# Performance work log

Measured on AMD Instinct MI355X. Metric: run time of the kernel, lower is better.

The kernel has to match this reference:

```python
import jax, jax.numpy as jnp
import numpy as np

B, CQ, CVK, L, H = 4, 256, 256, 2048, 8
D = CVK // H  # depth per head = 32
EPS = 1e-5    # BatchNorm eps


def setup_inputs() -> dict:
    key = jax.random.key(0)
    ks = jax.random.split(key, 32)
    n = lambda i, s, sc=1.0: jax.random.normal(ks[i], s, dtype=jnp.float32) * sc
    u = lambda i, s: jax.random.uniform(ks[i], s, dtype=jnp.float32, minval=0.5, maxval=1.5)
    inp = {
        'v': n(0, (B, CVK, L)), 'k': n(1, (B, CVK, L)), 'q': n(2, (B, CQ, L)),
        # trainable positional encodings (pe_q: image_shape_q, pe_vk: image_shape_vk)
        'pe_q': n(3, (CQ, L)), 'pe_vk': n(4, (CVK, L)),
        # W_query / W_key / W_value: Conv1d(kernel=1) weight [out,in] + bias, then BatchNorm1d (eval mode)
        'wq': n(5, (CVK, CQ), 0.05), 'bq': n(6, (CVK,), 0.05),
        'gq': 1.0 + n(7, (CVK,), 0.1), 'betaq': n(8, (CVK,), 0.1), 'mq': n(9, (CVK,), 0.1), 'varq': u(10, (CVK,)),
        'wk': n(11, (CVK, CVK), 0.05), 'bk': n(12, (CVK,), 0.05),
        'gk': 1.0 + n(13, (CVK,), 0.1), 'betak': n(14, (CVK,), 0.1), 'mk': n(15, (CVK,), 0.1), 'vark': u(16, (CVK,)),
        'wv': n(17, (CVK, CVK), 0.05), 'bv': n(18, (CVK,), 0.05),
        'gv': 1.0 + n(19, (CVK,), 0.1), 'betav': n(20, (CVK,), 0.1), 'mv': n(21, (CVK,), 0.1), 'varv': u(22, (CVK,)),
        # out_proj (zero-init in original; randomized here so gradients are non-trivial)
        'wo': n(23, (CQ, CVK), 0.05), 'bo': n(24, (CQ,), 0.05),
    }
    return inp


def _conv1(x, w, b):  # 1x1 conv == channel matmul: [b,c,l] -> [b,o,l]
    return jnp.einsum('oc,bcl->bol', w, x) + b[None, :, None]


def _bn(x, g, beta, mean, var):  # eval-mode BatchNorm1d over channel dim
    scale = g / jnp.sqrt(var + EPS)
    return (x - mean[:, None]) * scale[:, None] + beta[:, None]


def _mha(v, k, q, pe_q, pe_vk, wq, bq, gq, betaq, mq, varq,
         wk, bk, gk, betak, mk, vark, wv, bv, gv, betav, mv, varv, wo, bo):
    q_orig = q
    b = q.shape[0]
    vv = v + pe_vk[None]
    kk = k + pe_vk[None]
    qq = q + pe_q[None]
    qp = _bn(_conv1(qq, wq, bq), gq, betaq, mq, varq)   # [b, CVK, L]
    kp = _bn(_conv1(kk, wk, bk), gk, betak, mk, vark)
    vp = _bn(_conv1(vv, wv, bv), gv, betav, mv, varv)
    # split heads: [b, H, D, L]
    qh = qp.reshape(b, H, D, -1)
    kh = kp.reshape(b, H, D, -1)
    vh = vp.reshape(b, H, D, -1)
    # scaled dot-product attention over sequence dim (l: query pos, m: key pos)
    scores = jnp.einsum('bhdl,bhdm->bhlm', qh, kh) / jnp.sqrt(jnp.float32(D))
    p = jax.nn.softmax(scores, axis=-1)
    a = jnp.einsum('bhlm,bhdm->bhdl', p, vh)            # [b, H, D, L]
    a = a.reshape(b, H * D, -1)                          # [b, CVK, L]
    out = _conv1(a, wo, bo)                              # [b, CQ, L]
    return q_orig + out


def reference(v, k, q, pe_q, pe_vk, wq, bq, gq, betaq, mq, varq,
              wk, bk, gk, betak, mk, vark, wv, bv, gv, betav, mv, varv, wo, bo):
    return _mha(v, k, q, pe_q, pe_vk, wq, bq, gq, betaq, mq, varq,
                wk, bk, gk, betak, mk, vark, wv, bv, gv, betav, mv, varv, wo, bo)
```

## Files before the change

### kernel.cpp

```cpp
#include <hip/hip_runtime.h>
#include <hip/hip_bf16.h>

#define BB 4
#define CC 256
#define LL 2048
#define HH 8
#define DD 32
#define EPSV 1e-5f

typedef __bf16 bf16x8 __attribute__((ext_vector_type(8)));
typedef __bf16 bf16x4 __attribute__((ext_vector_type(4)));
typedef __bf16 bf16x2 __attribute__((ext_vector_type(2)));
typedef float  f32x4  __attribute__((ext_vector_type(4)));
typedef float  f32x16 __attribute__((ext_vector_type(16)));
typedef unsigned int u32x4 __attribute__((ext_vector_type(4)));

static __device__ __forceinline__ unsigned pkbf(float lo, float hi) {
    bf16x2 p; p[0] = (__bf16)lo; p[1] = (__bf16)hi;
    return __builtin_bit_cast(unsigned, p);
}

__global__ __launch_bounds__(256) void prep_kernel(
    const float* __restrict__ qin, const float* __restrict__ kin,
    const float* __restrict__ vin, const float* __restrict__ peq,
    const float* __restrict__ pevk,
    __bf16* __restrict__ xq, __bf16* __restrict__ xk, __bf16* __restrict__ xv,
    const float* __restrict__ wq, const float* __restrict__ bq,
    const float* __restrict__ gq, const float* __restrict__ betaq,
    const float* __restrict__ mq, const float* __restrict__ varq,
    const float* __restrict__ wk, const float* __restrict__ bk,
    const float* __restrict__ gk, const float* __restrict__ betak,
    const float* __restrict__ mk, const float* __restrict__ vark,
    const float* __restrict__ wv, const float* __restrict__ bv,
    const float* __restrict__ gv, const float* __restrict__ betav,
    const float* __restrict__ mv, const float* __restrict__ varv,
    const float* __restrict__ wo,
    __bf16* __restrict__ wqb, __bf16* __restrict__ wkb,
    __bf16* __restrict__ wvb, __bf16* __restrict__ wob,
    float* __restrict__ bqf, float* __restrict__ bkf, float* __restrict__ bvf,
    float qscale)
{
    __shared__ __align__(16) float xs[64][66];
    const int t = threadIdx.x;

    if (blockIdx.z == 12) {
        const int which = blockIdx.y;
        const float* w    = which==0?wq:(which==1?wk:(which==2?wv:wo));
        const float* bias = which==0?bq:(which==1?bk:bv);
        const float* g    = which==0?gq:(which==1?gk:gv);
        const float* beta = which==0?betaq:(which==1?betak:betav);
        const float* mean = which==0?mq:(which==1?mk:mv);
        const float* var  = which==0?varq:(which==1?vark:varv);
        __bf16* wout = which==0?wqb:(which==1?wkb:(which==2?wvb:wob));
        float*  bout = which==0?bqf:(which==1?bkf:bvf);
        const float extra = (which==0) ? qscale : 1.0f;

        const int base = blockIdx.x * 2048;
        for (int i = 0; i < 8; ++i) {
            const int idx = base + i * 256 + t;
            const int o = idx >> 8;
            const float sc = (which < 3) ? (g[o] * rsqrtf(var[o] + EPSV) * extra) : 1.0f;
            wout[idx] = (__bf16)(w[idx] * sc);
        }
        if (blockIdx.x == 0 && which < 3) {
            const int o = t;
            const float sc = g[o] * rsqrtf(var[o] + EPSV);
            bout[o] = ((bias[o] - mean[o]) * sc + beta[o]) * extra;
        }
        return;
    }

    const int lt = blockIdx.x * 64;
    const int ct = blockIdx.y * 64;
    const int z  = blockIdx.z;
    const int b  = z & 3;
    const int which = z >> 2;

    const float* xin = which == 0 ? qin : (which == 1 ? kin : vin);
    const float* pe  = which == 0 ? peq : pevk;
    __bf16* xout     = which == 0 ? xq  : (which == 1 ? xk : xv);

    for (int i = 0; i < 8; ++i) {
        const int idx = i * 256 + t;
        const int row = idx >> 5;
        const int lch = idx & 31;
        const float2 xv2 = *(const float2*)&xin[(size_t)(b * CC + ct + row) * LL + lt + lch * 2];
        const float2 pv2 = *(const float2*)&pe[(size_t)(ct + row) * LL + lt + lch * 2];
        float2 s; s.x = xv2.x + pv2.x; s.y = xv2.y + pv2.y;
        *(float2*)&xs[row][lch * 2] = s;
    }
    __syncthreads();

    for (int i = 0; i < 2; ++i) {
        const int idx = i * 256 + t;
        const int lrow = idx >> 3;
        const int ch   = idx & 7;
        bf16x8 v;
        #pragma unroll
        for (int j = 0; j < 8; ++j) v[j] = (__bf16)xs[ch * 8 + j][lrow];
        *(bf16x8*)&xout[(size_t)(b * LL + lt + lrow) * CC + ct + ch * 8] = v;
    }
}

__global__ __launch_bounds__(512) void qkv_gemm_kernel(
    const __bf16* __restrict__ wqb, const __bf16* __restrict__ wkb,
    const __bf16* __restrict__ wvb,
    const __bf16* __restrict__ xq, const __bf16* __restrict__ xk,
    const __bf16* __restrict__ xv,
    const float* __restrict__ bqf, const float* __restrict__ bkf,
    const float* __restrict__ bvf,
    __bf16* __restrict__ qTo, __bf16* __restrict__ kTo, __bf16* __restrict__ vNo)
{
    __shared__ __align__(16) __bf16 Wl[64][136];
    __shared__ __align__(16) __bf16 Xl[128][136];
    __bf16 (*Tl)[72] = (__bf16(*)[72])Xl;

    const int z = blockIdx.z;
    const int which = z >> 2;
    const int b = z & 3;
    const __bf16* W    = which==0 ? wqb : (which==1 ? wkb : wvb);
    const __bf16* X    = which==0 ? xq  : (which==1 ? xk  : xv);
    const float*  bias = which==0 ? bqf : (which==1 ? bkf : bvf);

    const int lt = blockIdx.x * 128;
    const int ot = blockIdx.y * 64;
    const int t  = threadIdx.x;
    const int wv = t >> 6;
    const int wm = wv >> 2;
    const int wn = wv & 3;
    const int l  = t & 63;
    const int lq = l & 15;
    const int g  = l >> 4;

    f32x4 acc[2][2];
    #pragma unroll
    for (int mi = 0; mi < 2; ++mi)
        #pragma unroll
        for (int ni = 0; ni < 2; ++ni) acc[mi][ni] = (f32x4){0.f,0.f,0.f,0.f};

    for (int ks = 0; ks < 2; ++ks) {
        __syncthreads();
        #pragma unroll
        for (int i = 0; i < 2; ++i) {
            const int idx = i * 512 + t;
            const int row = idx >> 4, ch = idx & 15;
            *(bf16x8*)&Wl[row][ch * 8] =
                *(const bf16x8*)&W[(size_t)(ot + row) * CC + ks * 128 + ch * 8];
        }
        #pragma unroll
        for (int i = 0; i < 4; ++i) {
            const int idx = i * 512 + t;
            const int row = idx >> 4, ch = idx & 15;
            *(bf16x8*)&Xl[row][ch * 8] =
                *(const bf16x8*)&X[(size_t)(b * LL + lt + row) * CC + ks * 128 + ch * 8];
        }
        __syncthreads();

        #pragma unroll
        for (int kk = 0; kk < 4; ++kk) {
            bf16x8 af[2], bfr[2];
            #pragma unroll
            for (int mi = 0; mi < 2; ++mi)
                af[mi] = *(const bf16x8*)&Wl[wm * 32 + mi * 16 + lq][kk * 32 + g * 8];
            #pragma unroll
            for (int ni = 0; ni < 2; ++ni)
                bfr[ni] = *(const bf16x8*)&Xl[wn * 32 + ni * 16 + lq][kk * 32 + g * 8];
            #pragma unroll
            for (int mi = 0; mi < 2; ++mi)
                #pragma unroll
                for (int ni = 0; ni < 2; ++ni)
                    acc[mi][ni] = __builtin_amdgcn_mfma_f32_16x16x32_bf16(
                        af[mi], bfr[ni], acc[mi][ni], 0, 0, 0);
        }
    }

    if (which < 2) {
        __bf16* outT = which==0 ? qTo : kTo;
        __syncthreads();
        #pragma unroll
        for (int mi = 0; mi < 2; ++mi) {
            const float4 b4 = *(const float4*)&bias[ot + wm * 32 + mi * 16 + g * 4];
            #pragma unroll
            for (int ni = 0; ni < 2; ++ni) {
                bf16x4 pv;
                pv[0] = (__bf16)(acc[mi][ni][0] + b4.x);
                pv[1] = (__bf16)(acc[mi][ni][1] + b4.y);
                pv[2] = (__bf16)(acc[mi][ni][2] + b4.z);
                pv[3] = (__bf16)(acc[mi][ni][3] + b4.w);
                *(bf16x4*)&Tl[wn * 32 + ni * 16 + lq][wm * 32 + mi * 16 + g * 4] = pv;
            }
        }
        __syncthreads();
        #pragma unroll
        for (int i = 0; i < 2; ++i) {
            const int idx = i * 512 + t;
            const int lrow = idx >> 3, ch = idx & 7;
            *(bf16x8*)&outT[(size_t)(b * LL + lt + lrow) * CC + ot + ch * 8] =
                *(const bf16x8*)&Tl[lrow][ch * 8];
        }
    } else {
        #pragma unroll
        for (int mi = 0; mi < 2; ++mi) {
            const float4 b4 = *(const float4*)&bias[ot + wm * 32 + mi * 16 + g * 4];
            const float bb[4] = {b4.x, b4.y, b4.z, b4.w};
            #pragma unroll
            for (int ni = 0; ni < 2; ++ni) {
                const int col = lt + wn * 32 + ni * 16 + lq;
                #pragma unroll
                for (int r = 0; r < 4; ++r) {
                    const int o = ot + wm * 32 + mi * 16 + g * 4 + r;
                    vNo[(size_t)(b * CC + o) * LL + col] = (__bf16)(acc[mi][ni][r] + bb[r]);
                }
            }
        }
    }
}

__global__ __launch_bounds__(256) void attn_mfma_kernel(
    const __bf16* __restrict__ qT, const __bf16* __restrict__ kT,
    const __bf16* __restrict__ vN, __bf16* __restrict__ aT)
{
    __shared__ __align__(16) __bf16 KB[2][128 * 32];
    __shared__ __align__(16) __bf16 VB[2][32 * 128];

    const int qb = blockIdx.x;
    const int h  = blockIdx.y;
    const int b  = blockIdx.z;
    const int t  = threadIdx.x;
    const int w  = t >> 6;
    const int l  = t & 63;
    const int lq = l & 31;
    const int hi = l >> 5;

    const int q0 = qb * 128 + w * 32;

    const __bf16* qrow = qT + ((size_t)(b * LL) + q0 + lq) * CC + h * DD;
    const bf16x8 qf0 = *(const bf16x8*)&qrow[hi * 8];
    const bf16x8 qf1 = *(const bf16x8*)&qrow[16 + hi * 8];

    const __bf16* kTb = kT + (size_t)(b * LL) * CC + h * DD;
    const __bf16* vNb = vN + ((size_t)(b * CC) + h * DD) * LL;

    const int s0 = t, s1 = 256 + t;
    const int sk0 = s0 >> 2, sp0 = s0 & 3;
    const int sk1 = s1 >> 2, sp1 = s1 & 3;
    const int sd0 = s0 >> 4, sv0 = s0 & 15;
    const int sd1 = s1 >> 4, sv1 = s1 & 15;
    const int kw0 = sk0 * 32 + (sp0 ^ ((sk0 >> 1) & 3)) * 8;
    const int kw1 = sk1 * 32 + (sp1 ^ ((sk1 >> 1) & 3)) * 8;
    const int vw0 = sd0 * 128 + (sv0 ^ (sd0 & 7)) * 8;
    const int vw1 = sd1 * 128 + (sv1 ^ (sd1 & 7)) * 8;

    bf16x8 kr0, kr1, vr0, vr1;
    #define LOADREGS(KT0) \
        kr0 = *(const bf16x8*)&kTb[(size_t)((KT0) + sk0) * CC + sp0 * 8]; \
        kr1 = *(const bf16x8*)&kTb[(size_t)((KT0) + sk1) * CC + sp1 * 8]; \
        vr0 = *(const bf16x8*)&vNb[(size_t)sd0 * LL + (KT0) + sv0 * 8];   \
        vr1 = *(const bf16x8*)&vNb[(size_t)sd1 * LL + (KT0) + sv1 * 8];
    #define WRITEBUF(BUF) \
        *(bf16x8*)&KB[BUF][kw0] = kr0; *(bf16x8*)&KB[BUF][kw1] = kr1; \
        *(bf16x8*)&VB[BUF][vw0] = vr0; *(bf16x8*)&VB[BUF][vw1] = vr1;

    LOADREGS(0)
    WRITEBUF(0)
    LOADREGS(128)

    f32x16 O;
    #pragma unroll
    for (int r = 0; r < 16; ++r) O[r] = 0.f;
    float ssum = 0.f;

    const int NT = LL / 128;
    for (int it = 0; it < NT; ++it) {
        const int buf = it & 1;
        __syncthreads();
        const __bf16* KBb = KB[buf];
        const __bf16* VBb = VB[buf];

        #pragma unroll
        for (int kb = 0; kb < 128; kb += 32) {
            const int key = kb + lq;
            const int ksw = (key >> 1) & 3;
            f32x16 S;
            #pragma unroll
            for (int r = 0; r < 16; ++r) S[r] = 0.f;
            {
                const bf16x8 kf0 = *(const bf16x8*)&KBb[key * 32 + ((hi    ) ^ ksw) * 8];
                const bf16x8 kf1 = *(const bf16x8*)&KBb[key * 32 + ((2 + hi) ^ ksw) * 8];
                __builtin_amdgcn_s_setprio(1);
                S = __builtin_amdgcn_mfma_f32_32x32x16_bf16(kf0, qf0, S, 0, 0, 0);
                S = __builtin_amdgcn_mfma_f32_32x32x16_bf16(kf1, qf1, S, 0, 0, 0);
                __builtin_amdgcn_s_setprio(0);
            }
            float e[16];
            #pragma unroll
            for (int r = 0; r < 16; ++r) e[r] = __builtin_amdgcn_exp2f(S[r]);
            float s = 0.f;
            #pragma unroll
            for (int r = 0; r < 16; r += 4) s += (e[r] + e[r+1]) + (e[r+2] + e[r+3]);
            ssum += s;
            unsigned a[8];
            #pragma unroll
            for (int i = 0; i < 8; ++i) a[i] = pkbf(e[2*i], e[2*i+1]);
            #pragma unroll
            for (int c = 0; c < 2; ++c) {
                unsigned w0 = a[4*c+0], w1 = a[4*c+1], w2 = a[4*c+2], w3 = a[4*c+3];
                asm volatile("v_permlane32_swap_b32 %0, %1" : "+v"(w0), "+v"(w2));
                asm volatile("v_permlane32_swap_b32 %0, %1" : "+v"(w1), "+v"(w3));
                u32x4 pv4 = {w0, w1, w2, w3};
                const bf16x8 pf = __builtin_bit_cast(bf16x8, pv4);
                const int slot = (kb >> 3) + 2 * c + hi;
                const bf16x8 vf = *(const bf16x8*)&VBb[lq * 128 + (slot ^ (lq & 7)) * 8];
                __builtin_amdgcn_s_setprio(1);
                O = __builtin_amdgcn_mfma_f32_32x32x16_bf16(vf, pf, O, 0, 0, 0);
                __builtin_amdgcn_s_setprio(0);
            }
        }

        if (it + 1 < NT) { WRITEBUF(buf ^ 1) }
        if (it + 2 < NT) { LOADREGS((it + 2) * 128) }
    }
    #undef LOADREGS
    #undef WRITEBUF

    ssum += __shfl_xor(ssum, 32);
    const float inv = 1.f / ssum;

    __bf16* arow = aT + ((size_t)(b * LL) + q0 + lq) * CC + h * DD;
    #pragma unroll
    for (int gi = 0; gi < 4; ++gi) {
        bf16x4 ov;
        #pragma unroll
        for (int r = 0; r < 4; ++r) ov[r] = (__bf16)(O[4*gi + r] * inv);
        *(bf16x4*)&arow[8 * gi + 4 * hi] = ov;
    }
}

__global__ __launch_bounds__(256) void outproj_kernel(
    const __bf16* __restrict__ W, const __bf16* __restrict__ X,
    const float* __restrict__ bias, const float* __restrict__ resid,
    float* __restrict__ outF)
{
    __shared__ __align__(16) __bf16 Wl[64][136];
    __shared__ __align__(16) __bf16 Xl[64][136];

    const int lt = blockIdx.x * 64;
    const int ot = blockIdx.y * 64;
    const int b  = blockIdx.z;
    const int t  = threadIdx.x;
    const int wv = t >> 6;
    const int wm = wv >> 1;
    const int wn = wv & 1;
    const int l  = t & 63;
    const int lq = l & 15;
    const int g  = l >> 4;

    f32x4 acc[2][2];
    #pragma unroll
    for (int mi = 0; mi < 2; ++mi)
        #pragma unroll
        for (int ni = 0; ni < 2; ++ni) acc[mi][ni] = (f32x4){0.f,0.f,0.f,0.f};

    for (int ks = 0; ks < 2; ++ks) {
        __syncthreads();
        #pragma unroll
        for (int i = 0; i < 4; ++i) {
            const int idx = i * 256 + t;
            const int row = idx >> 4, ch = idx & 15;
            *(bf16x8*)&Wl[row][ch * 8] =
                *(const bf16x8*)&W[(size_t)(ot + row) * CC + ks * 128 + ch * 8];
        }
        #pragma unroll
        for (int i = 0; i < 4; ++i) {
            const int idx = i * 256 + t;
            const int row = idx >> 4, ch = idx & 15;
            *(bf16x8*)&Xl[row][ch * 8] =
                *(const bf16x8*)&X[(size_t)(b * LL + lt + row) * CC + ks * 128 + ch * 8];
        }
        __syncthreads();

        #pragma unroll
        for (int kk = 0; kk < 4; ++kk) {
            bf16x8 af[2], bfr[2];
            #pragma unroll
            for (int mi = 0; mi < 2; ++mi)
                af[mi] = *(const bf16x8*)&Wl[wm * 32 + mi * 16 + lq][kk * 32 + g * 8];
            #pragma unroll
            for (int ni = 0; ni < 2; ++ni)
                bfr[ni] = *(const bf16x8*)&Xl[wn * 32 + ni * 16 + lq][kk * 32 + g * 8];
            #pragma unroll
            for (int mi = 0; mi < 2; ++mi)
                #pragma unroll
                for (int ni = 0; ni < 2; ++ni)
                    acc[mi][ni] = __builtin_amdgcn_mfma_f32_16x16x32_bf16(
                        af[mi], bfr[ni], acc[mi][ni], 0, 0, 0);
        }
    }

    #pragma unroll
    for (int mi = 0; mi < 2; ++mi) {
        const float4 b4 = *(const float4*)&bias[ot + wm * 32 + mi * 16 + g * 4];
        const float bb[4] = {b4.x, b4.y, b4.z, b4.w};
        #pragma unroll
        for (int ni = 0; ni < 2; ++ni) {
            const int col = lt + wn * 32 + ni * 16 + lq;
            #pragma unroll
            for (int r = 0; r < 4; ++r) {
                const int o = ot + wm * 32 + mi * 16 + g * 4 + r;
                const size_t a = (size_t)(b * CC + o) * LL + col;
                outF[a] = acc[mi][ni][r] + bb[r] + resid[a];
            }
        }
    }
}

extern "C" void kernel_launch(void* const* d_in, const int* in_sizes, int n_in,
                              void* d_out, int out_size, void* d_ws, size_t ws_size,
                              hipStream_t stream)
{
    const float* v     = (const float*)d_in[0];
    const float* k     = (const float*)d_in[1];
    const float* q     = (const float*)d_in[2];
    const float* pe_q  = (const float*)d_in[3];
    const float* pe_vk = (const float*)d_in[4];
    const float* wq    = (const float*)d_in[5];
    const float* bq    = (const float*)d_in[6];
    const float* gq    = (const float*)d_in[7];
    const float* betaq = (const float*)d_in[8];
    const float* mq    = (const float*)d_in[9];
    const float* varq  = (const float*)d_in[10];
    const float* wk    = (const float*)d_in[11];
    const float* bk    = (const float*)d_in[12];
    const float* gk    = (const float*)d_in[13];
    const float* betak = (const float*)d_in[14];
    const float* mk    = (const float*)d_in[15];
    const float* vark  = (const float*)d_in[16];
    const float* wv    = (const float*)d_in[17];
    const float* bv    = (const float*)d_in[18];
    const float* gv    = (const float*)d_in[19];
    const float* betav = (const float*)d_in[20];
    const float* mv    = (const float*)d_in[21];
    const float* varv  = (const float*)d_in[22];
    const float* wo    = (const float*)d_in[23];
    const float* bo    = (const float*)d_in[24];

    float* out = (float*)d_out;

    const size_t E = (size_t)BB * CC * LL;
    __bf16* xq  = (__bf16*)d_ws;
    __bf16* xk  = xq + E;
    __bf16* xv  = xk + E;
    __bf16* qT  = xv + E;
    __bf16* kT  = qT + E;
    __bf16* vN  = kT + E;
    __bf16* aT  = vN + E;
    __bf16* wqb = aT + E;
    __bf16* wkb = wqb + 65536;
    __bf16* wvb = wkb + 65536;
    __bf16* wob = wvb + 65536;
    float*  bqf = (float*)(wob + 65536);
    float*  bkf = bqf + 256;
    float*  bvf = bkf + 256;

    const float qscale = 0.17677669529663687f * 1.4426950408889634f;

    hipLaunchKernelGGL(prep_kernel, dim3(32, 4, 13), dim3(256), 0, stream,
                       q, k, v, pe_q, pe_vk, xq, xk, xv,
                       wq, bq, gq, betaq, mq, varq,
                       wk, bk, gk, betak, mk, vark,
                       wv, bv, gv, betav, mv, varv,
                       wo, wqb, wkb, wvb, wob, bqf, bkf, bvf, qscale);

    hipLaunchKernelGGL(qkv_gemm_kernel, dim3(16, 4, 12), dim3(512), 0, stream,
                       wqb, wkb, wvb, xq, xk, xv, bqf, bkf, bvf, qT, kT, vN);

    hipLaunchKernelGGL(attn_mfma_kernel, dim3(16, HH, BB), dim3(256), 0, stream,
                       qT, kT, vN, aT);

    hipLaunchKernelGGL(outproj_kernel, dim3(32, 4, 4), dim3(256), 0, stream,
                       wob, aT, bo, q, out);
}
```

Baseline: 65.38 us.

## Fuse input prep and weight folding into QKV and out-proj GEMM loads

Removes the separate prep kernel. The QKV GEMM now reads fp32 inputs and positional encodings directly, adds and transposes them while staging into LDS, and folds the BatchNorm scale into the fp32 weights as it loads them. The bias fold is computed in the epilogue, and out-proj converts fp32 wo on the fly. This saves one launch and the bf16 intermediate write/read round trip. In exchange, each GEMM block redundantly re-reads and re-converts the weights and PE, and the strided fp32 column loads of X are less coalesced.

Measured after the change: 65.11 us. About the same (-0.4%).

```diff
diff --git a/kernel.cpp b/kernel.cpp
--- a/kernel.cpp
+++ b/kernel.cpp
@@ -20,11 +20,10 @@
     return __builtin_bit_cast(unsigned, p);
 }
 
-__global__ __launch_bounds__(256) void prep_kernel(
+__global__ __launch_bounds__(512) void qkv_gemm_kernel(
     const float* __restrict__ qin, const float* __restrict__ kin,
-    const float* __restrict__ vin, const float* __restrict__ peq,
-    const float* __restrict__ pevk,
-    __bf16* __restrict__ xq, __bf16* __restrict__ xk, __bf16* __restrict__ xv,
+    const float* __restrict__ vin,
+    const float* __restrict__ peq, const float* __restrict__ pevk,
     const float* __restrict__ wq, const float* __restrict__ bq,
     const float* __restrict__ gq, const float* __restrict__ betaq,
     const float* __restrict__ mq, const float* __restrict__ varq,
@@ -34,82 +33,8 @@
     const float* __restrict__ wv, const float* __restrict__ bv,
     const float* __restrict__ gv, const float* __restrict__ betav,
     const float* __restrict__ mv, const float* __restrict__ varv,
-    const float* __restrict__ wo,
-    __bf16* __restrict__ wqb, __bf16* __restrict__ wkb,
-    __bf16* __restrict__ wvb, __bf16* __restrict__ wob,
-    float* __restrict__ bqf, float* __restrict__ bkf, float* __restrict__ bvf,
+    __bf16* __restrict__ qTo, __bf16* __restrict__ kTo, __bf16* __restrict__ vNo,
     float qscale)
-{
-    __shared__ __align__(16) float xs[64][66];
-    const int t = threadIdx.x;
-
-    if (blockIdx.z == 12) {
-        const int which = blockIdx.y;
-        const float* w    = which==0?wq:(which==1?wk:(which==2?wv:wo));
-        const float* bias = which==0?bq:(which==1?bk:bv);
-        const float* g    = which==0?gq:(which==1?gk:gv);
-        const float* beta = which==0?betaq:(which==1?betak:betav);
-        const float* mean = which==0?mq:(which==1?mk:mv);
-        const float* var  = which==0?varq:(which==1?vark:varv);
-        __bf16* wout = which==0?wqb:(which==1?wkb:(which==2?wvb:wob));
-        float*  bout = which==0?bqf:(which==1?bkf:bvf);
-        const float extra = (which==0) ? qscale : 1.0f;
-
-        const int base = blockIdx.x * 2048;
-        for (int i = 0; i < 8; ++i) {
-            const int idx = base + i * 256 + t;
-            const int o = idx >> 8;
-            const float sc = (which < 3) ? (g[o] * rsqrtf(var[o] + EPSV) * extra) : 1.0f;
-            wout[idx] = (__bf16)(w[idx] * sc);
-        }
-        if (blockIdx.x == 0 && which < 3) {
-            const int o = t;
-            const float sc = g[o] * rsqrtf(var[o] + EPSV);
-            bout[o] = ((bias[o] - mean[o]) * sc + beta[o]) * extra;
-        }
-        return;
-    }
-
-    const int lt = blockIdx.x * 64;
-    const int ct = blockIdx.y * 64;
-    const int z  = blockIdx.z;
-    const int b  = z & 3;
-    const int which = z >> 2;
-
-    const float* xin = which == 0 ? qin : (which == 1 ? kin : vin);
-    const float* pe  = which == 0 ? peq : pevk;
-    __bf16* xout     = which == 0 ? xq  : (which == 1 ? xk : xv);
-
-    for (int i = 0; i < 8; ++i) {
-        const int idx = i * 256 + t;
-        const int row = idx >> 5;
-        const int lch = idx & 31;
-        const float2 xv2 = *(const float2*)&xin[(size_t)(b * CC + ct + row) * LL + lt + lch * 2];
-        const float2 pv2 = *(const float2*)&pe[(size_t)(ct + row) * LL + lt + lch * 2];
-        float2 s; s.x = xv2.x + pv2.x; s.y = xv2.y + pv2.y;
-        *(float2*)&xs[row][lch * 2] = s;
-    }
-    __syncthreads();
-
-    for (int i = 0; i < 2; ++i) {
-        const int idx = i * 256 + t;
-        const int lrow = idx >> 3;
-        const int ch   = idx & 7;
-        bf16x8 v;
-        #pragma unroll
-        for (int j = 0; j < 8; ++j) v[j] = (__bf16)xs[ch * 8 + j][lrow];
-        *(bf16x8*)&xout[(size_t)(b * LL + lt + lrow) * CC + ct + ch * 8] = v;
-    }
-}
-
-__global__ __launch_bounds__(512) void qkv_gemm_kernel(
-    const __bf16* __restrict__ wqb, const __bf16* __restrict__ wkb,
-    const __bf16* __restrict__ wvb,
-    const __bf16* __restrict__ xq, const __bf16* __restrict__ xk,
-    const __bf16* __restrict__ xv,
-    const float* __restrict__ bqf, const float* __restrict__ bkf,
-    const float* __restrict__ bvf,
-    __bf16* __restrict__ qTo, __bf16* __restrict__ kTo, __bf16* __restrict__ vNo)
 {
     __shared__ __align__(16) __bf16 Wl[64][136];
     __shared__ __align__(16) __bf16 Xl[128][136];
@@ -118,16 +43,22 @@
     const int z = blockIdx.z;
     const int which = z >> 2;
     const int b = z & 3;
-    const __bf16* W    = which==0 ? wqb : (which==1 ? wkb : wvb);
-    const __bf16* X    = which==0 ? xq  : (which==1 ? xk  : xv);
-    const float*  bias = which==0 ? bqf : (which==1 ? bkf : bvf);
+    const float* X    = which==0 ? qin : (which==1 ? kin : vin);
+    const float* pe   = which==0 ? peq : pevk;
+    const float* W    = which==0 ? wq  : (which==1 ? wk  : wv);
+    const float* bia  = which==0 ? bq  : (which==1 ? bk  : bv);
+    const float* gam  = which==0 ? gq  : (which==1 ? gk  : gv);
+    const float* bet  = which==0 ? betaq : (which==1 ? betak : betav);
+    const float* mea  = which==0 ? mq  : (which==1 ? mk  : mv);
+    const float* var  = which==0 ? varq : (which==1 ? vark : varv);
+    const float extra = (which==0) ? qscale : 1.0f;
 
     const int lt = blockIdx.x * 128;
     const int ot = blockIdx.y * 64;
     const int t  = threadIdx.x;
-    const int wv = t >> 6;
-    const int wm = wv >> 2;
-    const int wn = wv & 3;
+    const int wvi = t >> 6;
+    const int wm = wvi >> 2;
+    const int wn = wvi & 3;
     const int l  = t & 63;
     const int lq = l & 15;
     const int g  = l >> 4;
@@ -141,18 +72,35 @@
     for (int ks = 0; ks < 2; ++ks) {
         __syncthreads();
         #pragma unroll
-        for (int i = 0; i < 2; ++i) {
-            const int idx = i * 512 + t;
-            const int row = idx >> 4, ch = idx & 15;
-            *(bf16x8*)&Wl[row][ch * 8] =
-                *(const bf16x8*)&W[(size_t)(ot + row) * CC + ks * 128 + ch * 8];
-        }
-        #pragma unroll
         for (int i = 0; i < 4; ++i) {
             const int idx = i * 512 + t;
-            const int row = idx >> 4, ch = idx & 15;
-            *(bf16x8*)&Xl[row][ch * 8] =
-                *(const bf16x8*)&X[(size_t)(b * LL + lt + row) * CC + ks * 128 + ch * 8];
+            const int row = idx >> 5;
+            const int ch  = idx & 31;
+            const int o   = ot + row;
+            const float sc = gam[o] * rsqrtf(var[o] + EPSV) * extra;
+            const float4 w4 = *(const float4*)&W[(size_t)o * CC + ks * 128 + ch * 4];
+            bf16x4 wb;
+            wb[0] = (__bf16)(w4.x * sc); wb[1] = (__bf16)(w4.y * sc);
+            wb[2] = (__bf16)(w4.z * sc); wb[3] = (__bf16)(w4.w * sc);
+            *(bf16x4*)&Wl[row][ch * 4] = wb;
+        }
+        #pragma unroll
+        for (int i = 0; i < 2; ++i) {
+            const int slot = i * 512 + t;
+            const int lp = slot & 63;
+            const int co = slot >> 6;
+            const float* xp = &X[(size_t)(b * CC + ks * 128 + co * 8) * LL + lt + lp * 2];
+            const float* pp = &pe[(size_t)(ks * 128 + co * 8) * LL + lt + lp * 2];
+            bf16x8 lo, hi;
+            #pragma unroll
+            for (int j = 0; j < 8; ++j) {
+                const float2 a = *(const float2*)&xp[(size_t)j * LL];
+                const float2 p = *(const float2*)&pp[(size_t)j * LL];
+                lo[j] = (__bf16)(a.x + p.x);
+                hi[j] = (__bf16)(a.y + p.y);
+            }
+            *(bf16x8*)&Xl[lp * 2    ][co * 8] = lo;
+            *(bf16x8*)&Xl[lp * 2 + 1][co * 8] = hi;
         }
         __syncthreads();
 
@@ -174,19 +122,37 @@
         }
     }
 
+    float bb[2][4];
+    #pragma unroll
+    for (int mi = 0; mi < 2; ++mi) {
+        const int o4 = ot + wm * 32 + mi * 16 + g * 4;
+        const float4 b4 = *(const float4*)&bia[o4];
+        const float4 g4 = *(const float4*)&gam[o4];
+        const float4 v4 = *(const float4*)&var[o4];
+        const float4 m4 = *(const float4*)&mea[o4];
+        const float4 t4 = *(const float4*)&bet[o4];
+        const float bs[4] = {b4.x,b4.y,b4.z,b4.w};
+        const float gs[4] = {g4.x,g4.y,g4.z,g4.w};
+        const float vs[4] = {v4.x,v4.y,v4.z,v4.w};
+        const float ms[4] = {m4.x,m4.y,m4.z,m4.w};
+        const float ts[4] = {t4.x,t4.y,t4.z,t4.w};
+        #pragma unroll
+        for (int r = 0; r < 4; ++r) {
+            const float sc = gs[r] * rsqrtf(vs[r] + EPSV);
+            bb[mi][r] = ((bs[r] - ms[r]) * sc + ts[r]) * extra;
+        }
+    }
+
     if (which < 2) {
         __bf16* outT = which==0 ? qTo : kTo;
         __syncthreads();
         #pragma unroll
         for (int mi = 0; mi < 2; ++mi) {
-            const float4 b4 = *(const float4*)&bias[ot + wm * 32 + mi * 16 + g * 4];
             #pragma unroll
             for (int ni = 0; ni < 2; ++ni) {
                 bf16x4 pv;
-                pv[0] = (__bf16)(acc[mi][ni][0] + b4.x);
-                pv[1] = (__bf16)(acc[mi][ni][1] + b4.y);
-                pv[2] = (__bf16)(acc[mi][ni][2] + b4.z);
-                pv[3] = (__bf16)(acc[mi][ni][3] + b4.w);
+                #pragma unroll
+                for (int r = 0; r < 4; ++r) pv[r] = (__bf16)(acc[mi][ni][r] + bb[mi][r]);
                 *(bf16x4*)&Tl[wn * 32 + ni * 16 + lq][wm * 32 + mi * 16 + g * 4] = pv;
             }
         }
@@ -201,15 +167,13 @@
     } else {
         #pragma unroll
         for (int mi = 0; mi < 2; ++mi) {
-            const float4 b4 = *(const float4*)&bias[ot + wm * 32 + mi * 16 + g * 4];
-            const float bb[4] = {b4.x, b4.y, b4.z, b4.w};
             #pragma unroll
             for (int ni = 0; ni < 2; ++ni) {
                 const int col = lt + wn * 32 + ni * 16 + lq;
                 #pragma unroll
                 for (int r = 0; r < 4; ++r) {
                     const int o = ot + wm * 32 + mi * 16 + g * 4 + r;
-                    vNo[(size_t)(b * CC + o) * LL + col] = (__bf16)(acc[mi][ni][r] + bb[r]);
+                    vNo[(size_t)(b * CC + o) * LL + col] = (__bf16)(acc[mi][ni][r] + bb[mi][r]);
                 }
             }
         }
@@ -337,7 +301,7 @@
 }
 
 __global__ __launch_bounds__(256) void outproj_kernel(
-    const __bf16* __restrict__ W, const __bf16* __restrict__ X,
+    const float* __restrict__ W, const __bf16* __restrict__ X,
     const float* __restrict__ bias, const float* __restrict__ resid,
     float* __restrict__ outF)
 {
@@ -348,9 +312,9 @@
     const int ot = blockIdx.y * 64;
     const int b  = blockIdx.z;
     const int t  = threadIdx.x;
-    const int wv = t >> 6;
-    const int wm = wv >> 1;
-    const int wn = wv & 1;
+    const int wvi = t >> 6;
+    const int wm = wvi >> 1;
+    const int wn = wvi & 1;
     const int l  = t & 63;
     const int lq = l & 15;
     const int g  = l >> 4;
@@ -364,11 +328,15 @@
     for (int ks = 0; ks < 2; ++ks) {
         __syncthreads();
         #pragma unroll
-        for (int i = 0; i < 4; ++i) {
+        for (int i = 0; i < 8; ++i) {
             const int idx = i * 256 + t;
-            const int row = idx >> 4, ch = idx & 15;
-            *(bf16x8*)&Wl[row][ch * 8] =
-                *(const bf16x8*)&W[(size_t)(ot + row) * CC + ks * 128 + ch * 8];
+            const int row = idx >> 5;
+            const int ch  = idx & 31;
+            const float4 w4 = *(const float4*)&W[(size_t)(ot + row) * CC + ks * 128 + ch * 4];
+            bf16x4 wb;
+            wb[0] = (__bf16)w4.x; wb[1] = (__bf16)w4.y;
+            wb[2] = (__bf16)w4.z; wb[3] = (__bf16)w4.w;
+            *(bf16x4*)&Wl[row][ch * 4] = wb;
         }
         #pragma unroll
         for (int i = 0; i < 4; ++i) {
@@ -447,36 +415,23 @@
     float* out = (float*)d_out;
 
     const size_t E = (size_t)BB * CC * LL;
-    __bf16* xq  = (__bf16*)d_ws;
-    __bf16* xk  = xq + E;
-    __bf16* xv  = xk + E;
-    __bf16* qT  = xv + E;
+    __bf16* qT  = (__bf16*)d_ws;
     __bf16* kT  = qT + E;
     __bf16* vN  = kT + E;
     __bf16* aT  = vN + E;
-    __bf16* wqb = aT + E;
-    __bf16* wkb = wqb + 65536;
-    __bf16* wvb = wkb + 65536;
-    __bf16* wob = wvb + 65536;
-    float*  bqf = (float*)(wob + 65536);
-    float*  bkf = bqf + 256;
-    float*  bvf = bkf + 256;
 
     const float qscale = 0.17677669529663687f * 1.4426950408889634f;
 
-    hipLaunchKernelGGL(prep_kernel, dim3(32, 4, 13), dim3(256), 0, stream,
-                       q, k, v, pe_q, pe_vk, xq, xk, xv,
+    hipLaunchKernelGGL(qkv_gemm_kernel, dim3(16, 4, 12), dim3(512), 0, stream,
+                       q, k, v, pe_q, pe_vk,
                        wq, bq, gq, betaq, mq, varq,
                        wk, bk, gk, betak, mk, vark,
                        wv, bv, gv, betav, mv, varv,
-                       wo, wqb, wkb, wvb, wob, bqf, bkf, bvf, qscale);
-
-    hipLaunchKernelGGL(qkv_gemm_kernel, dim3(16, 4, 12), dim3(512), 0, stream,
-                       wqb, wkb, wvb, xq, xk, xv, bqf, bkf, bvf, qT, kT, vN);
+                       qT, kT, vN, qscale);
 
     hipLaunchKernelGGL(attn_mfma_kernel, dim3(16, HH, BB), dim3(256), 0, stream,
                        qT, kT, vN, aT);
 
     hipLaunchKernelGGL(outproj_kernel, dim3(32, 4, 4), dim3(256), 0, stream,
-                       wob, aT, bo, q, out);
+                       wo, aT, bo, q, out);
 }
```
